# Performance work log

Hardware: AMD Instinct MI355X
Metric: run time of the kernel (lower is better)

## Reference

```python
import jax, jax.numpy as jnp
import numpy as np

HEADS = 4
DIM_HEAD = 32
SCALE = DIM_HEAD ** -0.5
EPS = 1e-5


def setup_inputs() -> dict:
    key = jax.random.key(0)
    ks = jax.random.split(key, 5)
    b, c, h, w = 32, 256, 64, 64
    hidden = HEADS * DIM_HEAD  # 128
    return {
        "x": jax.random.normal(ks[0], (b, c, h, w), dtype=jnp.float32),
        "Wqkv": jax.random.normal(ks[1], (3 * hidden, c), dtype=jnp.float32) * 0.05,
        "bqkv": jax.random.normal(ks[2], (3 * hidden,), dtype=jnp.float32) * 0.05,
        "Wout": jax.random.normal(ks[3], (c, hidden), dtype=jnp.float32) * 0.05,
        "bout": jax.random.normal(ks[4], (c,), dtype=jnp.float32) * 0.05,
        "gamma": jnp.ones((c,), dtype=jnp.float32),
        "beta": jnp.zeros((c,), dtype=jnp.float32),
    }


def reference(x, Wqkv, bqkv, Wout, bout, gamma, beta):
    b, c, h, w = x.shape
    n = h * w
    # 1x1 conv == per-pixel linear: [b,c,h,w] x [3*hidden,c] -> [b,3*hidden,h,w]
    qkv = jnp.einsum('bchw,oc->bohw', x, Wqkv) + bqkv[None, :, None, None]
    q, k, v = jnp.split(qkv, 3, axis=1)
    # b (heads dh) x y -> b heads dh n
    q = q.reshape(b, HEADS, DIM_HEAD, n)
    k = k.reshape(b, HEADS, DIM_HEAD, n)
    v = v.reshape(b, HEADS, DIM_HEAD, n)
    q = jax.nn.softmax(q, axis=-2) * SCALE  # softmax over dim_head axis
    k = jax.nn.softmax(k, axis=-2)
    context = jnp.einsum('bhdn,bhen->bhde', k, v)   # [b,h,dh,dh]
    out = jnp.einsum('bhde,bhdn->bhen', context, q)  # [b,h,dh,n]
    out = out.reshape(b, HEADS * DIM_HEAD, h, w)
    # 1x1 conv projection back to dim
    out = jnp.einsum('bchw,oc->bohw', out, Wout) + bout[None, :, None, None]
    # GroupNorm(1, dim): normalize over (C,H,W) per sample, affine per channel
    mu = jnp.mean(out, axis=(1, 2, 3), keepdims=True)
    var = jnp.var(out, axis=(1, 2, 3), keepdims=True)
    out = (out - mu) * jax.lax.rsqrt(var + EPS)
    return out * gamma[None, :, None, None] + beta[None, :, None, None]
```

## Files before the change

kernel.cpp:

```cpp
#include <hip/hip_runtime.h>
#include <math.h>


#define NPIX 4096
#define SCALE 0.17677669529663687f

typedef __bf16 bf16;
typedef __bf16 bf16x4 __attribute__((ext_vector_type(4)));
typedef __bf16 bf16x8 __attribute__((ext_vector_type(8)));
typedef float  f32x4  __attribute__((ext_vector_type(4)));

__global__ __launch_bounds__(256) void k0_convert(
    const float* __restrict__ Wqkv, const float* __restrict__ Wout,
    bf16* __restrict__ wqkv_bf, bf16* __restrict__ wout_bf)
{
    int i = blockIdx.x * 256 + threadIdx.x;
    if (i < 98304) wqkv_bf[i] = (bf16)Wqkv[i];
    else           wout_bf[i - 98304] = (bf16)Wout[i - 98304];
}

__global__ __launch_bounds__(256, 4) void k1_qkv(
    const float* __restrict__ x, const bf16* __restrict__ wqkv_bf,
    const float* __restrict__ bqkv, bf16* __restrict__ q_wsT,
    bf16* __restrict__ part)
{
    __shared__ __align__(16) bf16 sm[18432];
    bf16* xT = sm;

    const int blk  = blockIdx.x;
    const int b    = blk >> 6;
    const int n0   = (blk & 63) << 6;
    const int tid  = threadIdx.x;
    const int lane = tid & 63;
    const int s    = __builtin_amdgcn_readfirstlane(tid >> 6);
    const int m16  = lane & 15;
    const int quad = lane >> 4;

    const float* xb = x + (size_t)b * (256 * NPIX) + n0;
    {
        const int px  = tid & 63;
        const int cq0 = tid >> 6;
        float vv[16][4];
        #pragma unroll
        for (int it = 0; it < 16; ++it) {
            const float* xp = xb + (size_t)(cq0 + 4*it) * 4 * NPIX + px;
            vv[it][0] = xp[0];
            vv[it][1] = xp[NPIX];
            vv[it][2] = xp[2*NPIX];
            vv[it][3] = xp[3*NPIX];
        }
        #pragma unroll
        for (int it = 0; it < 16; ++it) {
            int cq = cq0 + 4*it;
            int g  = cq >> 1;
            int o  = (cq & 1) * 4;
            int gp = g ^ (px & 7);
            bf16x4 pk = { (bf16)vv[it][0], (bf16)vv[it][1],
                          (bf16)vv[it][2], (bf16)vv[it][3] };
            *(bf16x4*)&xT[px*256 + gp*8 + o] = pk;
        }
    }
    __syncthreads();

    {
        f32x4 qacc[2][4] = {};
        for (int kc = 0; kc < 8; ++kc) {
            bf16x8 bfr[4];
            #pragma unroll
            for (int nt = 0; nt < 4; ++nt) {
                int px = nt*16 + m16;
                int gp = (kc*4 + quad) ^ (px & 7);
                bfr[nt] = *(const bf16x8*)&xT[px*256 + gp*8];
            }
            #pragma unroll
            for (int mt = 0; mt < 2; ++mt) {
                int row = s*32 + mt*16 + m16;
                bf16x8 afr = *(const bf16x8*)&wqkv_bf[(size_t)row*256 + kc*32 + quad*8];
                #pragma unroll
                for (int nt = 0; nt < 4; ++nt)
                    qacc[mt][nt] = __builtin_amdgcn_mfma_f32_16x16x32_bf16(afr, bfr[nt], qacc[mt][nt], 0, 0, 0);
            }
        }
        float bq[8];
        #pragma unroll
        for (int j = 0; j < 8; ++j)
            bq[j] = bqkv[s*32 + (j >> 2)*16 + quad*4 + (j & 3)];

        #pragma unroll
        for (int nt = 0; nt < 4; ++nt) {
            float v[8]; float mx = -1e30f;
            #pragma unroll
            for (int j = 0; j < 8; ++j) { v[j] = qacc[j>>2][nt][j&3] + bq[j]; mx = fmaxf(mx, v[j]); }
            mx = fmaxf(mx, __shfl_xor(mx, 16));
            mx = fmaxf(mx, __shfl_xor(mx, 32));
            float sum = 0.f;
            #pragma unroll
            for (int j = 0; j < 8; ++j) { v[j] = __expf(v[j] - mx); sum += v[j]; }
            sum += __shfl_xor(sum, 16);
            sum += __shfl_xor(sum, 32);
            float rs = SCALE / sum;
            size_t rowb = (size_t)(b*4096 + n0 + nt*16 + m16) * 128;
            #pragma unroll
            for (int mt = 0; mt < 2; ++mt) {
                bf16x4 pk = { (bf16)(v[mt*4+0]*rs), (bf16)(v[mt*4+1]*rs),
                              (bf16)(v[mt*4+2]*rs), (bf16)(v[mt*4+3]*rs) };
                *(bf16x4*)&q_wsT[rowb + s*32 + mt*16 + quad*4] = pk;
            }
        }
    }

    f32x4 acc[4][4] = {};
    for (int kc = 0; kc < 8; ++kc) {
        bf16x8 bfr[4];
        #pragma unroll
        for (int nt = 0; nt < 4; ++nt) {
            int px = nt*16 + m16;
            int gp = (kc*4 + quad) ^ (px & 7);
            bfr[nt] = *(const bf16x8*)&xT[px*256 + gp*8];
        }
        #pragma unroll
        for (int mt = 0; mt < 4; ++mt) {
            int row = 128 + (mt >> 1)*128 + s*32 + (mt & 1)*16 + m16;
            bf16x8 afr = *(const bf16x8*)&wqkv_bf[(size_t)row*256 + kc*32 + quad*8];
            #pragma unroll
            for (int nt = 0; nt < 4; ++nt)
                acc[mt][nt] = __builtin_amdgcn_mfma_f32_16x16x32_bf16(afr, bfr[nt], acc[mt][nt], 0, 0, 0);
        }
    }

    float bk[8], bv[8];
    #pragma unroll
    for (int j = 0; j < 8; ++j) {
        int rr = (j >> 2)*16 + quad*4 + (j & 3);
        bk[j] = bqkv[128 + s*32 + rr];
        bv[j] = bqkv[256 + s*32 + rr];
    }

    __syncthreads();
    bf16* kl = sm + s*2304;
    bf16* vl = sm + 9216 + s*2304;
    #pragma unroll
    for (int nt = 0; nt < 4; ++nt) {
        float v[8]; float mx = -1e30f;
        #pragma unroll
        for (int j = 0; j < 8; ++j) { v[j] = acc[j>>2][nt][j&3] + bk[j]; mx = fmaxf(mx, v[j]); }
        mx = fmaxf(mx, __shfl_xor(mx, 16));
        mx = fmaxf(mx, __shfl_xor(mx, 32));
        float sum = 0.f;
        #pragma unroll
        for (int j = 0; j < 8; ++j) { v[j] = __expf(v[j] - mx); sum += v[j]; }
        sum += __shfl_xor(sum, 16);
        sum += __shfl_xor(sum, 32);
        float rs = 1.f / sum;
        #pragma unroll
        for (int j = 0; j < 8; ++j) {
            int d  = (j>>2)*16 + quad*4 + (j&3);
            int px = nt*16 + m16;
            kl[d*72 + px] = (bf16)(v[j] * rs);
            vl[d*72 + px] = (bf16)(acc[2 + (j>>2)][nt][j&3] + bv[j]);
        }
    }
    __syncthreads();

    f32x4 cacc[2][2] = {};
    #pragma unroll
    for (int ks = 0; ks < 2; ++ks) {
        bf16x8 ak[2], bvv[2];
        #pragma unroll
        for (int mt = 0; mt < 2; ++mt)
            ak[mt] = *(const bf16x8*)&kl[(mt*16 + m16)*72 + ks*32 + quad*8];
        #pragma unroll
        for (int nt = 0; nt < 2; ++nt)
            bvv[nt] = *(const bf16x8*)&vl[(nt*16 + m16)*72 + ks*32 + quad*8];
        #pragma unroll
        for (int mt = 0; mt < 2; ++mt)
            #pragma unroll
            for (int nt = 0; nt < 2; ++nt)
                cacc[mt][nt] = __builtin_amdgcn_mfma_f32_16x16x32_bf16(ak[mt], bvv[nt], cacc[mt][nt], 0, 0, 0);
    }
    bf16* pdst = part + (size_t)blk * 4096 + s*1024;
    #pragma unroll
    for (int mt = 0; mt < 2; ++mt)
        #pragma unroll
        for (int nt = 0; nt < 2; ++nt)
            #pragma unroll
            for (int r = 0; r < 4; ++r)
                pdst[(mt*16 + quad*4 + r)*32 + nt*16 + m16] = (bf16)cacc[mt][nt][r];
}

__global__ __launch_bounds__(256) void k2_reduce(
    const bf16* __restrict__ part, bf16* __restrict__ ctxT_bf)
{
    int i = blockIdx.x * 256 + threadIdx.x;
    int b = i >> 12, r = i & 4095;
    const bf16* p = part + (size_t)b * 64 * 4096 + r;
    float sum = 0.f;
    #pragma unroll 8
    for (int j = 0; j < 64; ++j) sum += (float)p[(size_t)j * 4096];
    int h = r >> 10, d = (r >> 5) & 31, e = r & 31;
    ctxT_bf[(size_t)((b*4 + h)*32 + e)*32 + d] = (bf16)sum;
}

__global__ __launch_bounds__(256) void k3_out(
    const bf16* __restrict__ q_wsT, const bf16* __restrict__ ctxT_bf,
    const bf16* __restrict__ wout_bf, const float* __restrict__ bout,
    float* __restrict__ out, float* __restrict__ gstats)
{
    __shared__ __align__(16) bf16 attnT[8192];
    __shared__ float red[512];
    const int blk  = blockIdx.x;
    const int b    = blk >> 6;
    const int n0   = (blk & 63) << 6;
    const int tid  = threadIdx.x;
    const int lane = tid & 63;
    const int s    = __builtin_amdgcn_readfirstlane(tid >> 6);
    const int m16  = lane & 15;
    const int quad = lane >> 4;

    f32x4 aacc[2][4] = {};
    {
        bf16x8 afr[2], bfr[4];
        const bf16* ctxs = ctxT_bf + (size_t)(b*4 + s) * 1024;
        #pragma unroll
        for (int mt = 0; mt < 2; ++mt)
            afr[mt] = *(const bf16x8*)&ctxs[(mt*16 + m16)*32 + quad*8];
        const bf16* qb = q_wsT + (size_t)(b*4096 + n0) * 128 + s*32;
        #pragma unroll
        for (int nt = 0; nt < 4; ++nt)
            bfr[nt] = *(const bf16x8*)&qb[(size_t)(nt*16 + m16)*128 + quad*8];
        #pragma unroll
        for (int mt = 0; mt < 2; ++mt)
            #pragma unroll
            for (int nt = 0; nt < 4; ++nt)
                aacc[mt][nt] = __builtin_amdgcn_mfma_f32_16x16x32_bf16(afr[mt], bfr[nt], aacc[mt][nt], 0, 0, 0);
    }

    #pragma unroll
    for (int mt = 0; mt < 2; ++mt)
        #pragma unroll
        for (int nt = 0; nt < 4; ++nt) {
            int p   = nt*16 + m16;
            int chb = s*32 + mt*16 + quad*4;
            int gp  = (chb >> 3) ^ m16;
            bf16x4 pk = { (bf16)aacc[mt][nt][0], (bf16)aacc[mt][nt][1],
                          (bf16)aacc[mt][nt][2], (bf16)aacc[mt][nt][3] };
            *(bf16x4*)&attnT[p*128 + gp*8 + (quad & 1)*4] = pk;
        }
    __syncthreads();

    f32x4 acc[4][4] = {};
    const bf16* wb = wout_bf + (size_t)s * 64 * 128;
    for (int kc = 0; kc < 4; ++kc) {
        bf16x8 wfr[4], xfr[4];
        #pragma unroll
        for (int mt = 0; mt < 4; ++mt)
            wfr[mt] = *(const bf16x8*)&wb[(size_t)(mt*16 + m16)*128 + kc*32 + quad*8];
        #pragma unroll
        for (int nt = 0; nt < 4; ++nt) {
            int p  = nt*16 + m16;
            int gp = (kc*4 + quad) ^ m16;
            xfr[nt] = *(const bf16x8*)&attnT[p*128 + gp*8];
        }
        #pragma unroll
        for (int mt = 0; mt < 4; ++mt)
            #pragma unroll
            for (int nt = 0; nt < 4; ++nt)
                acc[mt][nt] = __builtin_amdgcn_mfma_f32_16x16x32_bf16(wfr[mt], xfr[nt], acc[mt][nt], 0, 0, 0);
    }

    float ls = 0.f, lss = 0.f;
    float* ob = out + ((size_t)b*256 + s*64) * NPIX + n0;
    #pragma unroll
    for (int mt = 0; mt < 4; ++mt) {
        #pragma unroll
        for (int r = 0; r < 4; ++r) {
            int o = mt*16 + quad*4 + r;
            float bo = bout[s*64 + o];
            #pragma unroll
            for (int nt = 0; nt < 4; ++nt) {
                float v = acc[mt][nt][r] + bo;
                ob[(size_t)o*NPIX + nt*16 + m16] = v;
                ls += v; lss += v*v;
            }
        }
    }

    red[tid] = ls; red[256 + tid] = lss;
    __syncthreads();
    for (int off = 128; off > 0; off >>= 1) {
        if (tid < off) {
            red[tid]       += red[tid + off];
            red[256 + tid] += red[256 + tid + off];
        }
        __syncthreads();
    }
    if (tid == 0) {
        atomicAdd(&gstats[b],      red[0]);
        atomicAdd(&gstats[32 + b], red[256]);
    }
}

__global__ void k4_stats(float* __restrict__ gstats)
{
    int t = threadIdx.x;
    if (t < 32) {
        const float inv_cnt = 1.0f / 1048576.0f;
        float m   = gstats[t] * inv_cnt;
        float var = gstats[32 + t] * inv_cnt - m*m;
        gstats[64 + t] = m;
        gstats[96 + t] = rsqrtf(var + 1e-5f);
    }
}

__global__ __launch_bounds__(256) void k5_norm(
    float* __restrict__ out, const float* __restrict__ gstats,
    const float* __restrict__ gamma, const float* __restrict__ beta)
{
    size_t gid  = (size_t)blockIdx.x * 256 + threadIdx.x;
    size_t base = gid * 4;
    int b = (int)(base >> 20);
    int o = (int)((base >> 12) & 255);
    float m   = gstats[64 + b];
    float inv = gstats[96 + b];
    float a = inv * gamma[o];
    float c = beta[o] - m * a;
    float4 v = ((float4*)out)[gid];
    v.x = v.x * a + c; v.y = v.y * a + c;
    v.z = v.z * a + c; v.w = v.w * a + c;
    ((float4*)out)[gid] = v;
}

extern "C" void kernel_launch(void* const* d_in, const int* in_sizes, int n_in,
                              void* d_out, int out_size, void* d_ws, size_t ws_size,
                              hipStream_t stream) {
    const float* x     = (const float*)d_in[0];
    const float* Wqkv  = (const float*)d_in[1];
    const float* bqkv  = (const float*)d_in[2];
    const float* Wout  = (const float*)d_in[3];
    const float* bout  = (const float*)d_in[4];
    const float* gamma = (const float*)d_in[5];
    const float* beta  = (const float*)d_in[6];
    float* out = (float*)d_out;
    float* ws  = (float*)d_ws;

    bf16*  q_wsT   = (bf16*)ws;
    bf16*  wqkv_bf = (bf16*)(ws + 8388608);
    bf16*  wout_bf = (bf16*)(ws + 8437760);
    bf16*  ctxT_bf = (bf16*)(ws + 8454144);
    bf16*  part    = (bf16*)(ws + 16777216);
    float* gstats  = ws + 25165824;

    hipMemsetAsync(gstats, 0, 64 * sizeof(float), stream);
    k0_convert<<<512,  256, 0, stream>>>(Wqkv, Wout, wqkv_bf, wout_bf);
    k1_qkv    <<<2048, 256, 0, stream>>>(x, wqkv_bf, bqkv, q_wsT, part);
    k2_reduce <<<512,  256, 0, stream>>>(part, ctxT_bf);
    k3_out    <<<2048, 256, 0, stream>>>(q_wsT, ctxT_bf, wout_bf, bout, out, gstats);
    k4_stats  <<<1,     64, 0, stream>>>(gstats);
    k5_norm   <<<32768,256, 0, stream>>>(out, gstats, gamma, beta);
}
```

Baseline: 368.9 us.

## Tune occupancy bounds, split out-projection accumulators, fold stats into norm kernel

k1 launch bounds are relaxed from 4 to 3 waves and a sched_barrier is placed after the x loads. k3 gains a min-occupancy hint of 4 and computes its output projection in two 32-channel halves, which halves the live accumulator registers. The separate one-thread-block stats kernel is removed: the normalization kernel now derives mean and rsqrt inline and runs as a grid-stride loop with fewer blocks. This saves one launch and raises occupancy, at the cost of redundant stats math per element and possible lost load overlap in k1.

```diff
diff --git a/kernel.cpp b/kernel.cpp
--- a/kernel.cpp
+++ b/kernel.cpp
@@ -19,7 +19,7 @@
     else           wout_bf[i - 98304] = (bf16)Wout[i - 98304];
 }
 
-__global__ __launch_bounds__(256, 4) void k1_qkv(
+__global__ __launch_bounds__(256, 3) void k1_qkv(
     const float* __restrict__ x, const bf16* __restrict__ wqkv_bf,
     const float* __restrict__ bqkv, bf16* __restrict__ q_wsT,
     bf16* __restrict__ part)
@@ -49,15 +49,14 @@
             vv[it][2] = xp[2*NPIX];
             vv[it][3] = xp[3*NPIX];
         }
+        __builtin_amdgcn_sched_barrier(0);
         #pragma unroll
         for (int it = 0; it < 16; ++it) {
             int cq = cq0 + 4*it;
-            int g  = cq >> 1;
-            int o  = (cq & 1) * 4;
-            int gp = g ^ (px & 7);
+            int gp = (cq >> 1) ^ (px & 7);
             bf16x4 pk = { (bf16)vv[it][0], (bf16)vv[it][1],
                           (bf16)vv[it][2], (bf16)vv[it][3] };
-            *(bf16x4*)&xT[px*256 + gp*8 + o] = pk;
+            *(bf16x4*)&xT[px*256 + gp*8 + (cq & 1)*4] = pk;
         }
     }
     __syncthreads();
@@ -201,7 +200,7 @@
     ctxT_bf[(size_t)((b*4 + h)*32 + e)*32 + d] = (bf16)sum;
 }
 
-__global__ __launch_bounds__(256) void k3_out(
+__global__ __launch_bounds__(256, 4) void k3_out(
     const bf16* __restrict__ q_wsT, const bf16* __restrict__ ctxT_bf,
     const bf16* __restrict__ wout_bf, const float* __restrict__ bout,
     float* __restrict__ out, float* __restrict__ gstats)
@@ -248,39 +247,42 @@
         }
     __syncthreads();
 
-    f32x4 acc[4][4] = {};
-    const bf16* wb = wout_bf + (size_t)s * 64 * 128;
-    for (int kc = 0; kc < 4; ++kc) {
-        bf16x8 wfr[4], xfr[4];
-        #pragma unroll
-        for (int mt = 0; mt < 4; ++mt)
-            wfr[mt] = *(const bf16x8*)&wb[(size_t)(mt*16 + m16)*128 + kc*32 + quad*8];
-        #pragma unroll
-        for (int nt = 0; nt < 4; ++nt) {
-            int p  = nt*16 + m16;
-            int gp = (kc*4 + quad) ^ m16;
-            xfr[nt] = *(const bf16x8*)&attnT[p*128 + gp*8];
-        }
-        #pragma unroll
-        for (int mt = 0; mt < 4; ++mt)
-            #pragma unroll
-            for (int nt = 0; nt < 4; ++nt)
-                acc[mt][nt] = __builtin_amdgcn_mfma_f32_16x16x32_bf16(wfr[mt], xfr[nt], acc[mt][nt], 0, 0, 0);
-    }
-
     float ls = 0.f, lss = 0.f;
     float* ob = out + ((size_t)b*256 + s*64) * NPIX + n0;
-    #pragma unroll
-    for (int mt = 0; mt < 4; ++mt) {
-        #pragma unroll
-        for (int r = 0; r < 4; ++r) {
-            int o = mt*16 + quad*4 + r;
-            float bo = bout[s*64 + o];
+    #pragma unroll 1
+    for (int h = 0; h < 2; ++h) {
+        f32x4 acc[2][4] = {};
+        const bf16* wb = wout_bf + (size_t)(s*64 + h*32) * 128;
+        for (int kc = 0; kc < 4; ++kc) {
+            bf16x8 wfr[2], xfr[4];
+            #pragma unroll
+            for (int mt = 0; mt < 2; ++mt)
+                wfr[mt] = *(const bf16x8*)&wb[(size_t)(mt*16 + m16)*128 + kc*32 + quad*8];
             #pragma unroll
             for (int nt = 0; nt < 4; ++nt) {
-                float v = acc[mt][nt][r] + bo;
-                ob[(size_t)o*NPIX + nt*16 + m16] = v;
-                ls += v; lss += v*v;
+                int p  = nt*16 + m16;
+                int gp = (kc*4 + quad) ^ m16;
+                xfr[nt] = *(const bf16x8*)&attnT[p*128 + gp*8];
+            }
+            #pragma unroll
+            for (int mt = 0; mt < 2; ++mt)
+                #pragma unroll
+                for (int nt = 0; nt < 4; ++nt)
+                    acc[mt][nt] = __builtin_amdgcn_mfma_f32_16x16x32_bf16(wfr[mt], xfr[nt], acc[mt][nt], 0, 0, 0);
+        }
+
+        #pragma unroll
+        for (int mt = 0; mt < 2; ++mt) {
+            #pragma unroll
+            for (int r = 0; r < 4; ++r) {
+                int o = h*32 + mt*16 + quad*4 + r;
+                float bo = bout[s*64 + o];
+                #pragma unroll
+                for (int nt = 0; nt < 4; ++nt) {
+                    float v = acc[mt][nt][r] + bo;
+                    ob[(size_t)o*NPIX + nt*16 + m16] = v;
+                    ls += v; lss += v*v;
+                }
             }
         }
     }
@@ -300,34 +302,26 @@
     }
 }
 
-__global__ void k4_stats(float* __restrict__ gstats)
-{
-    int t = threadIdx.x;
-    if (t < 32) {
-        const float inv_cnt = 1.0f / 1048576.0f;
-        float m   = gstats[t] * inv_cnt;
-        float var = gstats[32 + t] * inv_cnt - m*m;
-        gstats[64 + t] = m;
-        gstats[96 + t] = rsqrtf(var + 1e-5f);
-    }
-}
-
 __global__ __launch_bounds__(256) void k5_norm(
     float* __restrict__ out, const float* __restrict__ gstats,
     const float* __restrict__ gamma, const float* __restrict__ beta)
 {
-    size_t gid  = (size_t)blockIdx.x * 256 + threadIdx.x;
-    size_t base = gid * 4;
-    int b = (int)(base >> 20);
-    int o = (int)((base >> 12) & 255);
-    float m   = gstats[64 + b];
-    float inv = gstats[96 + b];
-    float a = inv * gamma[o];
-    float c = beta[o] - m * a;
-    float4 v = ((float4*)out)[gid];
-    v.x = v.x * a + c; v.y = v.y * a + c;
-    v.z = v.z * a + c; v.w = v.w * a + c;
-    ((float4*)out)[gid] = v;
+    const float inv_cnt = 1.0f / 1048576.0f;
+    for (size_t gid = (size_t)blockIdx.x * 256 + threadIdx.x;
+         gid < 8388608; gid += (size_t)gridDim.x * 256) {
+        size_t base = gid * 4;
+        int b = (int)(base >> 20);
+        int o = (int)((base >> 12) & 255);
+        float m   = gstats[b]      * inv_cnt;
+        float var = gstats[32 + b] * inv_cnt - m*m;
+        float inv = rsqrtf(var + 1e-5f);
+        float a = inv * gamma[o];
+        float c = beta[o] - m * a;
+        float4 v = ((float4*)out)[gid];
+        v.x = v.x * a + c; v.y = v.y * a + c;
+        v.z = v.z * a + c; v.w = v.w * a + c;
+        ((float4*)out)[gid] = v;
+    }
 }
 
 extern "C" void kernel_launch(void* const* d_in, const int* in_sizes, int n_in,
@@ -355,6 +349,5 @@
     k1_qkv    <<<2048, 256, 0, stream>>>(x, wqkv_bf, bqkv, q_wsT, part);
     k2_reduce <<<512,  256, 0, stream>>>(part, ctxT_bf);
     k3_out    <<<2048, 256, 0, stream>>>(q_wsT, ctxT_bf, wout_bf, bout, out, gstats);
-    k4_stats  <<<1,     64, 0, stream>>>(gstats);
-    k5_norm   <<<32768,256, 0, stream>>>(out, gstats, gamma, beta);
-}
+    k5_norm   <<<4096, 256, 0, stream>>>(out, gstats, gamma, beta);
+}
```

New measurement: 386.6 us. 4.8% more time.
